# Performance work log

Hardware: AMD Instinct MI355X
Metric: run time of the kernel (lower is better)

## Reference

```python
import jax, jax.numpy as jnp
import numpy as np

ALPHA = 1.0   # get_spike_fn('ArcTan', 1.0, 20.0)
WIDTH = 20.0

@jax.custom_vjp
def arctan_spike(x):
    # Heaviside forward, ArcTan surrogate gradient
    return (x > 0).astype(x.dtype)

def _spike_fwd(x):
    return arctan_spike(x), x

def _spike_bwd(x, g):
    return (g * ALPHA / (1.0 + (WIDTH * x) ** 2),)

arctan_spike.defvjp(_spike_fwd, _spike_bwd)

T, B, F = 2048, 64, 512  # seq_len, batch, features (input_groups=256 -> F=512)
TAU_SYN, TAU_MEM, V_THRESH, W_SCALE = 0.08, 0.03, 1.0, 0.4

def setup_inputs() -> dict:
    key = jax.random.key(0)
    x = jax.random.normal(key, (T, B, F), dtype=jnp.float32)
    # ff weight: block_diag of input_groups copies of 0.4*I2 == 0.4*I_F
    W = (W_SCALE * jnp.eye(F, dtype=jnp.float32))
    leak_i = jnp.full((F,), 1.0 - TAU_SYN, dtype=jnp.float32)
    leak_v = jnp.full((F,), 1.0 - TAU_MEM, dtype=jnp.float32)
    thresh = jnp.full((F,), V_THRESH, dtype=jnp.float32)
    return {"x": x, "W": W, "leak_i": leak_i, "leak_v": leak_v, "thresh": thresh}

def reference(x, W, leak_i, leak_v, thresh):
    Tn, Bn, Fn = x.shape
    i0 = jnp.zeros((Bn, Fn), dtype=x.dtype)
    v0 = jnp.zeros((Bn, Fn), dtype=x.dtype)
    z0 = jnp.zeros((Bn, Fn), dtype=x.dtype)

    def step(carry, xt):
        i, v, z = carry
        ff = xt @ W.T                      # [B,F] linear synapse (no bias)
        i_new = leak_i * i + ff            # leaky synaptic current
        v_new = leak_v * v * (1.0 - z) + i_new  # membrane, reset-to-zero on spike
        z_new = arctan_spike(v_new - thresh)
        return (i_new, v_new, z_new), z_new

    _, out = jax.lax.scan(step, (i0, v0, z0), x)
    return out  # [T, B, F]
```

## Files before the change

kernel.cpp:

```cpp
#include <hip/hip_runtime.h>


constexpr int T_STEPS = 2048;
constexpr int B_DIM   = 64;
constexpr int F_DIM   = 512;
constexpr int BF      = B_DIM * F_DIM;
constexpr int NPAIR   = BF / 2;
constexpr int CHUNK   = 32;
constexpr int NCHUNK  = T_STEPS / CHUNK;

__global__ __launch_bounds__(64, 1) void snn_scan_kernel(
    const float* __restrict__ x,
    const float* __restrict__ W,
    const float* __restrict__ leak_i,
    const float* __restrict__ leak_v,
    const float* __restrict__ thresh,
    float* __restrict__ out) {

    const int p  = blockIdx.x * 64 + threadIdx.x;
    const int e  = 2 * p;
    const int f0 = e & (F_DIM - 1);

    const float w00 = W[(f0    ) * F_DIM + f0    ];
    const float w01 = W[(f0    ) * F_DIM + f0 + 1];
    const float w10 = W[(f0 + 1) * F_DIM + f0    ];
    const float w11 = W[(f0 + 1) * F_DIM + f0 + 1];
    const float li0 = leak_i[f0],     li1 = leak_i[f0 + 1];
    const float lv0 = leak_v[f0],     lv1 = leak_v[f0 + 1];
    const float th0 = thresh[f0],     th1 = thresh[f0 + 1];

    float i0 = 0.0f, v0 = 0.0f, z0 = 0.0f;
    float i1 = 0.0f, v1 = 0.0f, z1 = 0.0f;

    const float2* xp = (const float2*)(x + e);
    float2*       op = (float2*)(out + e);

    float2 bufA[CHUNK], bufB[CHUNK];

    auto load_chunk = [&](const float2* ptr, float2 (&buf)[CHUNK]) {
        #pragma unroll
        for (int j = 0; j < CHUNK; ++j) buf[j] = ptr[j * NPAIR];
    };

    auto process_chunk = [&](float2 (&buf)[CHUNK], float2* o) {
        #pragma unroll
        for (int j = 0; j < CHUNK; ++j) {
            const float xe = buf[j].x;
            const float xo = buf[j].y;
            const float ff0 = __fadd_rn(__fmul_rn(w00, xe), __fmul_rn(w01, xo));
            const float ff1 = __fadd_rn(__fmul_rn(w10, xe), __fmul_rn(w11, xo));
            i0 = __fadd_rn(__fmul_rn(li0, i0), ff0);
            i1 = __fadd_rn(__fmul_rn(li1, i1), ff1);
            float vm0 = __fmul_rn(lv0, v0);
            float vm1 = __fmul_rn(lv1, v1);
            vm0 = (z0 > 0.0f) ? 0.0f : vm0;
            vm1 = (z1 > 0.0f) ? 0.0f : vm1;
            v0 = __fadd_rn(vm0, i0);
            v1 = __fadd_rn(vm1, i1);
            z0 = (v0 > th0) ? 1.0f : 0.0f;
            z1 = (v1 > th1) ? 1.0f : 0.0f;
            o[j * NPAIR] = make_float2(z0, z1);
        }
    };

    load_chunk(xp, bufA);
    for (int c = 0; c < NCHUNK; c += 2) {
        load_chunk(xp + (c + 1) * (CHUNK * NPAIR), bufB);
        process_chunk(bufA, op + c * (CHUNK * NPAIR));
        if (c + 2 < NCHUNK)
            load_chunk(xp + (c + 2) * (CHUNK * NPAIR), bufA);
        process_chunk(bufB, op + (c + 1) * (CHUNK * NPAIR));
    }
}

extern "C" void kernel_launch(void* const* d_in, const int* in_sizes, int n_in,
                              void* d_out, int out_size, void* d_ws, size_t ws_size,
                              hipStream_t stream) {
    const float* x      = (const float*)d_in[0];
    const float* W      = (const float*)d_in[1];
    const float* leak_i = (const float*)d_in[2];
    const float* leak_v = (const float*)d_in[3];
    const float* thresh = (const float*)d_in[4];
    float* out = (float*)d_out;

    snn_scan_kernel<<<dim3(NPAIR / 64), dim3(64), 0, stream>>>(
        x, W, leak_i, leak_v, thresh, out);
}
```

Before: 442.4 us.

## Deepen prefetch pipeline to four buffers with nontemporal loads/stores

Replaces the two-buffer, 32-step prefetch scheme with a four-buffer rotation of 16-step chunks, so three chunks of loads stay in flight while one is processed. Loads and stores of x and spikes now use nontemporal builtins to avoid polluting caches with streaming data. Launch bounds are relaxed to allow two blocks per CU. The aim is to hide more memory latency in this serial-per-thread scan, at the cost of the same register footprint spread over more buffers and more branch checks.

Result: no change. 436.2 us (-1.4%).

```diff
diff --git a/kernel.cpp b/kernel.cpp
--- a/kernel.cpp
+++ b/kernel.cpp
@@ -1,15 +1,17 @@
 #include <hip/hip_runtime.h>
 
+
+typedef float v2f __attribute__((ext_vector_type(2)));
 
 constexpr int T_STEPS = 2048;
 constexpr int B_DIM   = 64;
 constexpr int F_DIM   = 512;
 constexpr int BF      = B_DIM * F_DIM;
 constexpr int NPAIR   = BF / 2;
-constexpr int CHUNK   = 32;
+constexpr int CHUNK   = 16;
 constexpr int NCHUNK  = T_STEPS / CHUNK;
 
-__global__ __launch_bounds__(64, 1) void snn_scan_kernel(
+__global__ __launch_bounds__(64, 2) void snn_scan_kernel(
     const float* __restrict__ x,
     const float* __restrict__ W,
     const float* __restrict__ leak_i,
@@ -21,28 +23,31 @@
     const int e  = 2 * p;
     const int f0 = e & (F_DIM - 1);
 
-    const float w00 = W[(f0    ) * F_DIM + f0    ];
-    const float w01 = W[(f0    ) * F_DIM + f0 + 1];
-    const float w10 = W[(f0 + 1) * F_DIM + f0    ];
-    const float w11 = W[(f0 + 1) * F_DIM + f0 + 1];
-    const float li0 = leak_i[f0],     li1 = leak_i[f0 + 1];
-    const float lv0 = leak_v[f0],     lv1 = leak_v[f0 + 1];
-    const float th0 = thresh[f0],     th1 = thresh[f0 + 1];
+    const float w00 = W[(size_t)(f0    ) * F_DIM + f0    ];
+    const float w01 = W[(size_t)(f0    ) * F_DIM + f0 + 1];
+    const float w10 = W[(size_t)(f0 + 1) * F_DIM + f0    ];
+    const float w11 = W[(size_t)(f0 + 1) * F_DIM + f0 + 1];
+    const float li0 = leak_i[f0], li1 = leak_i[f0 + 1];
+    const float lv0 = leak_v[f0], lv1 = leak_v[f0 + 1];
+    const float th0 = thresh[f0], th1 = thresh[f0 + 1];
 
     float i0 = 0.0f, v0 = 0.0f, z0 = 0.0f;
     float i1 = 0.0f, v1 = 0.0f, z1 = 0.0f;
 
-    const float2* xp = (const float2*)(x + e);
-    float2*       op = (float2*)(out + e);
+    const v2f* xp = (const v2f*)(x + e);
+    v2f*       op = (v2f*)(out + e);
 
-    float2 bufA[CHUNK], bufB[CHUNK];
+    v2f bufA[CHUNK], bufB[CHUNK], bufC[CHUNK], bufD[CHUNK];
 
-    auto load_chunk = [&](const float2* ptr, float2 (&buf)[CHUNK]) {
+    auto load_chunk = [&](int c, v2f (&buf)[CHUNK]) {
+        const v2f* ptr = xp + (size_t)c * (CHUNK * NPAIR);
         #pragma unroll
-        for (int j = 0; j < CHUNK; ++j) buf[j] = ptr[j * NPAIR];
+        for (int j = 0; j < CHUNK; ++j)
+            buf[j] = __builtin_nontemporal_load(ptr + (size_t)j * NPAIR);
     };
 
-    auto process_chunk = [&](float2 (&buf)[CHUNK], float2* o) {
+    auto process_chunk = [&](int c, v2f (&buf)[CHUNK]) {
+        v2f* o = op + (size_t)c * (CHUNK * NPAIR);
         #pragma unroll
         for (int j = 0; j < CHUNK; ++j) {
             const float xe = buf[j].x;
@@ -59,17 +64,23 @@
             v1 = __fadd_rn(vm1, i1);
             z0 = (v0 > th0) ? 1.0f : 0.0f;
             z1 = (v1 > th1) ? 1.0f : 0.0f;
-            o[j * NPAIR] = make_float2(z0, z1);
+            v2f zv; zv.x = z0; zv.y = z1;
+            __builtin_nontemporal_store(zv, o + (size_t)j * NPAIR);
         }
     };
 
-    load_chunk(xp, bufA);
-    for (int c = 0; c < NCHUNK; c += 2) {
-        load_chunk(xp + (c + 1) * (CHUNK * NPAIR), bufB);
-        process_chunk(bufA, op + c * (CHUNK * NPAIR));
-        if (c + 2 < NCHUNK)
-            load_chunk(xp + (c + 2) * (CHUNK * NPAIR), bufA);
-        process_chunk(bufB, op + (c + 1) * (CHUNK * NPAIR));
+    load_chunk(0, bufA);
+    load_chunk(1, bufB);
+    load_chunk(2, bufC);
+    for (int c = 0; c < NCHUNK; c += 4) {
+        if (c + 3 < NCHUNK) load_chunk(c + 3, bufD);
+        process_chunk(c, bufA);
+        if (c + 4 < NCHUNK) load_chunk(c + 4, bufA);
+        process_chunk(c + 1, bufB);
+        if (c + 5 < NCHUNK) load_chunk(c + 5, bufB);
+        process_chunk(c + 2, bufC);
+        if (c + 6 < NCHUNK) load_chunk(c + 6, bufC);
+        process_chunk(c + 3, bufD);
     }
 }
 
```
